# Optimization experiments

Hardware: AMD Instinct MI355X
Metric: run time of the kernel (lower is better)

The kernel has to match this reference:

```python
import jax, jax.numpy as jnp
import numpy as np

B, T, H, N, V, E = 4, 128, 1024, 300, 50265, 4800


def setup_inputs() -> dict:
    key = jax.random.key(0)
    ks = jax.random.split(key, 20)
    s = 0.02
    inp = {
        "hidden_states": jax.random.normal(ks[0], (B, T, H), jnp.float32),
        "qt": jax.random.normal(ks[1], (B, T, H), jnp.float32),
        "token_embedding": jax.random.normal(ks[2], (B, T, H), jnp.float32),
        "edges": jax.random.randint(ks[3], (B, 2, E), 0, N),
        "nodeidx2bartidx": jax.random.randint(ks[4], (N,), 0, V),
        # Linear params stored as [in, out] (y = x @ W + b), same math as torch Linear.
        "Wg": jax.random.normal(ks[5], (2 * H, V), jnp.float32) * s,
        "bg": jnp.zeros((V,), jnp.float32),
        "Wh": jax.random.normal(ks[6], (H, H), jnp.float32) * s,
        "Ws": jax.random.normal(ks[7], (H, H), jnp.float32) * s,
        "Wx": jax.random.normal(ks[8], (H, H), jnp.float32) * s,
        "bx": jnp.zeros((H,), jnp.float32),
        "Wps": jax.random.normal(ks[9], (H, 1), jnp.float32) * s,
        "bps": jnp.zeros((1,), jnp.float32),
        "Wc": jax.random.normal(ks[10], (2 * H, N), jnp.float32) * s,
        "bc": jnp.zeros((N,), jnp.float32),
        "Wgg": jax.random.normal(ks[11], (2 * H, 1), jnp.float32) * s,
        "bgg": jnp.zeros((1,), jnp.float32),
        "Wmg": jax.random.normal(ks[12], (2 * H, 1), jnp.float32) * s,
        "bmg": jnp.zeros((1,), jnp.float32),
    }
    return inp


def reference(hidden_states, qt, token_embedding, edges, nodeidx2bartidx,
              Wg, bg, Wh, Ws, Wx, bx, Wps, bps, Wc, bc, Wgg, bgg, Wmg, bmg):
    b, t, h = hidden_states.shape
    n = Wc.shape[1]
    dt = hidden_states.dtype

    hq = jnp.concatenate([hidden_states, qt], axis=-1)          # [B,T,2H]
    gen_pro = hq @ Wg + bg                                       # [B,T,V]
    gen_feat = hidden_states @ Wh + qt @ Ws + (token_embedding @ Wx + bx)
    pro_switch = jax.nn.sigmoid(gen_feat @ Wps + bps)            # [B,T,1]
    qe = jnp.concatenate([qt, token_embedding], axis=-1)
    copy_pro = qe @ Wc + bc                                      # [B,T,N]
    gsem_gate = jax.nn.sigmoid(hq @ Wgg + bgg)                   # [B,T,1]
    memory_gate = jax.nn.sigmoid(hq @ Wmg + bmg)                 # [B,T,1]

    # dense per-example adjacency from COO edges (duplicates accumulate, as in sparse->dense)
    bidx = jnp.arange(b)[:, None]
    Graph = jnp.zeros((b, n, n), dt).at[bidx, edges[:, 0, :], edges[:, 1, :]].add(jnp.asarray(1.0, dt))

    # gated memory recurrence over time + graph propagation
    def step(m_prev, xs):
        cp_t, mg_t = xs                                          # [B,N], [B,1]
        m = cp_t * mg_t + m_prev * (1.0 - mg_t)
        g = jnp.einsum('bij,bj->bi', Graph, m)
        return m, g

    cp_tm = jnp.swapaxes(copy_pro, 0, 1)                         # [T,B,N]
    mg_tm = jnp.swapaxes(memory_gate, 0, 1)                      # [T,B,1]
    _, gsem_tm = jax.lax.scan(step, jnp.zeros((b, n), dt), (cp_tm, mg_tm))
    gsem = jnp.swapaxes(gsem_tm, 0, 1)                           # [B,T,N]

    pro_gsem = copy_pro * gsem_gate + gsem * (1.0 - gsem_gate)
    coverage = jax.nn.softmax(pro_gsem * pro_switch, axis=-1).sum(axis=1)  # [B,N]

    # scatter-add node distribution into vocab space
    gsem_pro = jnp.zeros_like(gen_pro).at[:, :, nodeidx2bartidx].add(pro_gsem)
    total_pro = gen_pro * (1.0 - pro_switch) + gsem_pro * pro_switch
    return total_pro, coverage, jnp.squeeze(pro_switch, axis=-1)
```

## Files before the change

kernel.cpp:

```cpp
#include <hip/hip_runtime.h>
#include <hip/hip_bf16.h>
#include <stdint.h>

#define B_ 4
#define T_ 128
#define H_ 1024
#define N_ 300
#define V_ 50265
#define E_ 4800
#define R_ (B_*T_)
#define GK 2048

#define U_OFF     0
#define PS_OFF    3080
#define GG_OFF    3592
#define MG_OFF    4104
#define Z_OFF     4616
#define M_OFF     (Z_OFF + R_*N_)
#define CP_OFF    (M_OFF + R_*N_)
#define GRAPH_OFF (CP_OFF + R_*N_)
#define COV_OFF   (GRAPH_OFF + B_*N_*N_)
#define FLAG_OFF  (COV_OFF + B_*N_)
#define ABF_OFF   ((FLAG_OFF + 4) & ~3)

#define OUT_COV ((size_t)R_*V_)
#define OUT_PS  (OUT_COV + (size_t)B_*N_)

typedef unsigned short ushort_t;
typedef __bf16 bf16x8 __attribute__((ext_vector_type(8)));
typedef float  f32x4  __attribute__((ext_vector_type(4)));
typedef unsigned short ushort8v __attribute__((ext_vector_type(8)));
typedef unsigned short ushort4v __attribute__((ext_vector_type(4)));
typedef float f32x4v __attribute__((ext_vector_type(4)));

__device__ __forceinline__ ushort_t f2bf(float f) {
    unsigned u = __float_as_uint(f);
    unsigned r = (u + 0x7fffu + ((u >> 16) & 1u)) >> 16;
    return (ushort_t)r;
}
template<bool BF> __device__ __forceinline__ float ldv(const void* p, size_t i) {
    if constexpr (BF) {
        unsigned u = ((unsigned)((const ushort_t*)p)[i]) << 16;
        return __uint_as_float(u);
    } else {
        return ((const float*)p)[i];
    }
}
template<bool BF> __device__ __forceinline__ void stv(void* p, size_t i, float v) {
    if constexpr (BF) ((ushort_t*)p)[i] = f2bf(v);
    else              ((float*)p)[i] = v;
}
__device__ __forceinline__ float sigm(float x) { return 1.0f / (1.0f + expf(-x)); }

__device__ __forceinline__ void gload_lds16(const ushort_t* g, ushort_t* l) {
    __builtin_amdgcn_global_load_lds(
        (const __attribute__((address_space(1))) unsigned int*)g,
        (__attribute__((address_space(3))) unsigned int*)l, 16, 0, 0);
}

__global__ void k_probe(const ushort_t* __restrict__ x, int* __restrict__ flag)
{
    if (threadIdx.x == 0 && blockIdx.x == 0) {
        int cnt = 0;
        for (int i = 0; i < 256; ++i) {
            const int e = (x[i] >> 7) & 0xff;
            cnt += (e >= 100 && e <= 140) ? 1 : 0;
        }
        *flag = (cnt > 200) ? 1 : 0;
    }
}

template<bool BF>
__global__ __launch_bounds__(256)
void k_prep(const int* __restrict__ flag, const void* __restrict__ hs,
            const void* __restrict__ qt, ushort_t* __restrict__ Abf)
{
    if (*flag != (BF ? 1 : 0)) return;
    const int g = blockIdx.x * 256 + threadIdx.x;
    const int r  = g >> 8;
    const int kc = (g & 255) * 8;
    const void* src = (kc < H_) ? hs : qt;
    const int k = kc & (H_ - 1);
    ushort8v o;
    #pragma unroll
    for (int p = 0; p < 8; ++p) o[p] = f2bf(ldv<BF>(src, (size_t)r*H_ + k + p));
    *(ushort8v*)(Abf + (size_t)r*GK + kc) = o;
}

template<bool BF>
__global__ __launch_bounds__(256)
void k_u(const int* __restrict__ flag,
         const void* __restrict__ Wh, const void* __restrict__ Wsm,
         const void* __restrict__ Wx, const void* __restrict__ bx,
         const void* __restrict__ Wps, const void* __restrict__ bps,
         float* __restrict__ u)
{
    if (*flag != (BF ? 1 : 0)) return;
    const int t = threadIdx.x, w = t >> 6, l = t & 63;
    const int row = blockIdx.x * 4 + w;
    if (row > 3072) return;
    float s = 0.f;
    if (row < 3072) {
        const void* W = (row < 1024) ? Wh : (row < 2048) ? Wsm : Wx;
        const size_t k = (size_t)(row & 1023);
        for (int h = l; h < H_; h += 64)
            s += ldv<BF>(W, k*H_ + h) * ldv<BF>(Wps, h);
    } else {
        for (int h = l; h < H_; h += 64)
            s += ldv<BF>(bx, h) * ldv<BF>(Wps, h);
    }
    for (int o = 32; o; o >>= 1) s += __shfl_down(s, o);
    if (l == 0) {
        if (row < 3072) u[row] = s;
        else            u[3072] = s + ldv<BF>(bps, 0);
    }
}

template<bool BF>
__global__ __launch_bounds__(256)
void k_rows(const int* __restrict__ flag,
            const void* __restrict__ hs, const void* __restrict__ qt,
            const void* __restrict__ te, const float* __restrict__ u,
            const void* __restrict__ Wgg, const void* __restrict__ bgg,
            const void* __restrict__ Wmg, const void* __restrict__ bmg,
            float* __restrict__ ps, float* __restrict__ gg, float* __restrict__ mg,
            void* __restrict__ out_ps)
{
    if (*flag != (BF ? 1 : 0)) return;
    const int r = blockIdx.x, t = threadIdx.x;
    const float* uh = u; const float* us = u + 1024; const float* ux = u + 2048;
    float s1 = 0.f, s2 = 0.f, s3 = 0.f;
    for (int k = t; k < H_; k += 256) {
        const float a = ldv<BF>(hs, (size_t)r*H_ + k);
        const float b = ldv<BF>(qt, (size_t)r*H_ + k);
        const float c = ldv<BF>(te, (size_t)r*H_ + k);
        s1 += a*uh[k] + b*us[k] + c*ux[k];
        s2 += a*ldv<BF>(Wgg, k) + b*ldv<BF>(Wgg, H_ + k);
        s3 += a*ldv<BF>(Wmg, k) + b*ldv<BF>(Wmg, H_ + k);
    }
    for (int o = 32; o; o >>= 1) {
        s1 += __shfl_down(s1, o); s2 += __shfl_down(s2, o); s3 += __shfl_down(s3, o);
    }
    __shared__ float red[3][4];
    const int w = t >> 6, l = t & 63;
    if (l == 0) { red[0][w] = s1; red[1][w] = s2; red[2][w] = s3; }
    __syncthreads();
    if (t == 0) {
        const float S1 = red[0][0]+red[0][1]+red[0][2]+red[0][3] + u[3072];
        const float S2 = red[1][0]+red[1][1]+red[1][2]+red[1][3] + ldv<BF>(bgg, 0);
        const float S3 = red[2][0]+red[2][1]+red[2][2]+red[2][3] + ldv<BF>(bmg, 0);
        const float p = sigm(S1);
        ps[r] = p; gg[r] = sigm(S2); mg[r] = sigm(S3);
        stv<BF>(out_ps, r, p);
    }
}

template<bool BF>
__global__ __launch_bounds__(256)
void k_gbig(const int* __restrict__ flag,
            const ushort_t* __restrict__ Abf, const void* __restrict__ Bm,
            const void* __restrict__ bias, const float* __restrict__ ps,
            void* __restrict__ outh)
{
    if (*flag != (BF ? 1 : 0)) return;
    constexpr int BN = 64, BK = 32, BKp = 40, STEPS = GK / BK;
    __shared__ ushort_t As[2][512 * BK];
    __shared__ ushort_t Bs[2][BN * BKp];
    const int t = threadIdx.x, w = t >> 6, l = t & 63;
    const int lr = l & 15, lq = l >> 4;
    const int bn0 = blockIdx.x * BN;
    const int wm = w * 128;

    const int nB = t & 63, kg = t >> 6;
    const int gnB = bn0 + nB;
    const size_t gnClamp = (size_t)((gnB < V_) ? gnB : (V_ - 1));
    const bool gnOk = (gnB < V_);

    const int aRow = l >> 2;
    const int aCsrc = (l & 3) ^ ((l >> 3) & 3);
    const ushort_t* AgBase = Abf + (size_t)wm * GK;

    float bv[8];
    f32x4 acc[8][4] = {};

    auto loadB = [&](int s) {
        const int k0 = s * BK + kg * 8;
        #pragma unroll
        for (int p = 0; p < 8; ++p) {
            const float v = ldv<BF>(Bm, (size_t)(k0 + p) * V_ + gnClamp);
            bv[p] = gnOk ? v : 0.f;
        }
    };
    auto storeB = [&](int buf) {
        ushort8v b0;
        #pragma unroll
        for (int p = 0; p < 8; ++p) b0[p] = f2bf(bv[p]);
        *(ushort8v*)(&Bs[buf][nB * BKp + kg * 8]) = b0;
    };
    auto stageA = [&](int s, int buf) {
        const int k0 = s * BK;
        #pragma unroll
        for (int i = 0; i < 8; ++i) {
            const int m = i * 16 + aRow;
            const ushort_t* g = AgBase + (size_t)m * GK + k0 + aCsrc * 8;
            ushort_t* lp = &As[buf][(wm + i * 16) * BK];
            gload_lds16(g, lp);
        }
    };
    auto compute = [&](int buf) {
        const int aswz = (lq ^ ((lr >> 1) & 3)) * 8;
        const ushort_t* a_rd = &As[buf][(wm + lr) * BK + aswz];
        const ushort_t* b_rd = &Bs[buf][lr * BKp + lq * 8];
        bf16x8 bfr[4];
        #pragma unroll
        for (int j = 0; j < 4; ++j) bfr[j] = *(const bf16x8*)(b_rd + j * 16 * BKp);
        #pragma unroll
        for (int i = 0; i < 8; ++i) {
            const bf16x8 af = *(const bf16x8*)(a_rd + i * 16 * BK);
            #pragma unroll
            for (int j = 0; j < 4; ++j)
                acc[i][j] = __builtin_amdgcn_mfma_f32_16x16x32_bf16(af, bfr[j], acc[i][j], 0, 0, 0);
        }
    };

    loadB(0);
    stageA(0, 0);
    storeB(0);
    __syncthreads();
    int cur = 0;
    for (int s = 0; s < STEPS; ++s) {
        const bool more = (s + 1 < STEPS);
        if (more) { loadB(s + 1); stageA(s + 1, cur ^ 1); }
        compute(cur);
        if (more) {
            storeB(cur ^ 1);
            __syncthreads();
            cur ^= 1;
        }
    }

    #pragma unroll
    for (int j = 0; j < 4; ++j) {
        const int gcol = bn0 + j * 16 + lr;
        if (gcol < V_) {
            const float bvv = ldv<BF>(bias, gcol);
            #pragma unroll
            for (int i = 0; i < 8; ++i) {
                #pragma unroll
                for (int r2 = 0; r2 < 4; ++r2) {
                    const int row = wm + i * 16 + lq * 4 + r2;
                    stv<BF>(outh, (size_t)row * V_ + gcol,
                            (acc[i][j][r2] + bvv) * (1.0f - ps[row]));
                }
            }
        }
    }
}

template<int GN_, bool BF>
__global__ __launch_bounds__(256)
void k_gemm(const int* __restrict__ flag,
            const void* __restrict__ A1, const void* __restrict__ A2,
            const void* __restrict__ Bm, const void* __restrict__ bias,
            float* __restrict__ outf)
{
    if (*flag != (BF ? 1 : 0)) return;
    constexpr int BM = 128, BN = 128, BK = 32, BKp = 40;
    __shared__ ushort_t As[BM*BK];
    __shared__ ushort_t Bs[BN*BKp];
    const int t = threadIdx.x;
    const int w = t >> 6, l = t & 63;
    const int lr = l & 15, lq = l >> 4;
    const int bn0 = blockIdx.x * BN;
    const int bm0 = blockIdx.y * BM;
    const int wm = (w >> 1) * 64, wn = (w & 1) * 64;

    const int steps = GK/BK/4;
    const int kbeg  = blockIdx.z * steps * BK;

    const int hB = t >> 7;
    const int nB = t & 127;
    const int gnB = bn0 + nB;
    const size_t gnClamp = (size_t)((gnB < GN_) ? gnB : (GN_-1));
    const bool gnOk = (gnB < GN_);

    f32x4 acc[4][4] = {};
    const ushort_t* a_rd = As + (wm + lr)*BK  + lq*8;
    const ushort_t* b_rd = Bs + (wn + lr)*BKp + lq*8;

    ushort8v aBufH[2]; f32x4v aBufF[4]; float bv[16];

    auto load_step = [&](int s) {
        const int k0 = kbeg + s*BK;
        const void* Asrc = (k0 < H_) ? A1 : A2;
        const int kk = k0 & (H_ - 1);
        if constexpr (BF) {
            #pragma unroll
            for (int p = 0; p < 2; ++p) {
                const int slot = p*256 + t, m = slot >> 2, sub = slot & 3;
                aBufH[p] = *(const ushort8v*)((const ushort_t*)Asrc +
                             (size_t)(bm0 + m)*H_ + kk + sub*8);
            }
        } else {
            #pragma unroll
            for (int p = 0; p < 4; ++p) {
                const int slot = p*256 + t, m = slot >> 3, sub = slot & 7;
                aBufF[p] = *(const f32x4v*)((const float*)Asrc +
                             (size_t)(bm0 + m)*H_ + kk + sub*4);
            }
        }
        #pragma unroll
        for (int p = 0; p < 16; ++p) {
            const int k = hB*16 + p;
            const float v = ldv<BF>(Bm, (size_t)(k0 + k)*GN_ + gnClamp);
            bv[p] = gnOk ? v : 0.f;
        }
    };

    auto store_step = [&]() {
        if constexpr (BF) {
            #pragma unroll
            for (int p = 0; p < 2; ++p) {
                const int slot = p*256 + t, m = slot >> 2, sub = slot & 3;
                *(ushort8v*)(As + m*BK + sub*8) = aBufH[p];
            }
        } else {
            #pragma unroll
            for (int p = 0; p < 4; ++p) {
                const int slot = p*256 + t, m = slot >> 3, sub = slot & 7;
                ushort4v h4;
                h4[0] = f2bf(aBufF[p][0]); h4[1] = f2bf(aBufF[p][1]);
                h4[2] = f2bf(aBufF[p][2]); h4[3] = f2bf(aBufF[p][3]);
                *(ushort4v*)(As + m*BK + sub*4) = h4;
            }
        }
        ushort8v b0, b1;
        #pragma unroll
        for (int p = 0; p < 8; ++p)  b0[p] = f2bf(bv[p]);
        #pragma unroll
        for (int p = 0; p < 8; ++p)  b1[p] = f2bf(bv[8+p]);
        *(ushort8v*)(Bs + nB*BKp + hB*16)     = b0;
        *(ushort8v*)(Bs + nB*BKp + hB*16 + 8) = b1;
    };

    load_step(0);
    for (int s = 0; s < steps; ++s) {
        __syncthreads();
        store_step();
        __syncthreads();
        if (s + 1 < steps) load_step(s + 1);

        bf16x8 af[4], bfr[4];
        #pragma unroll
        for (int i = 0; i < 4; ++i) af[i]  = *(const bf16x8*)(a_rd + i*16*BK);
        #pragma unroll
        for (int j = 0; j < 4; ++j) bfr[j] = *(const bf16x8*)(b_rd + j*16*BKp);
        #pragma unroll
        for (int i = 0; i < 4; ++i)
            #pragma unroll
            for (int j = 0; j < 4; ++j)
                acc[i][j] = __builtin_amdgcn_mfma_f32_16x16x32_bf16(af[i], bfr[j], acc[i][j], 0, 0, 0);
    }

    #pragma unroll
    for (int j = 0; j < 4; ++j) {
        const int gcol = bn0 + wn + j*16 + lr;
        if (gcol < GN_) {
            const float bvv = (blockIdx.z == 0) ? ldv<BF>(bias, gcol) : 0.0f;
            #pragma unroll
            for (int i = 0; i < 4; ++i)
                #pragma unroll
                for (int r2 = 0; r2 < 4; ++r2) {
                    const int row = bm0 + wm + i*16 + lq*4 + r2;
                    atomicAdd(outf + (size_t)row*GN_ + gcol, acc[i][j][r2] + bvv);
                }
        }
    }
}

__global__ void k_graph(const int* __restrict__ edges, float* __restrict__ Graph)
{
    const int gid = blockIdx.x * 256 + threadIdx.x;
    if (gid >= B_*E_) return;
    const int b = gid / E_, e = gid - b*E_;
    const int* eb = edges + (size_t)b * 2 * E_;
    const int i = eb[e], j = eb[E_ + e];
    atomicAdd(Graph + (size_t)b*N_*N_ + (size_t)j*N_ + i, 1.0f);
}

__global__ void k_scan(const float* __restrict__ cp, const float* __restrict__ mg,
                       float* __restrict__ M)
{
    const int gid = blockIdx.x * 256 + threadIdx.x;
    if (gid >= B_*N_) return;
    const int b = gid / N_, n = gid - b*N_;
    float m = 0.f;
    for (int tt = 0; tt < T_; ++tt) {
        const int r = b*T_ + tt;
        const float g = mg[r];
        m = cp[(size_t)r*N_ + n]*g + m*(1.f - g);
        M[(size_t)r*N_ + n] = m;
    }
}

__global__ __launch_bounds__(320)
void k_gsem(const float* __restrict__ Graph, const float* __restrict__ M,
            const float* __restrict__ cp, const float* __restrict__ gg,
            const float* __restrict__ ps, float* __restrict__ z,
            float* __restrict__ cov)
{
    const int r = blockIdx.x;
    const int b = r >> 7;
    const int t = threadIdx.x, w = t >> 6, l = t & 63;
    __shared__ float ml[N_];
    __shared__ float red[5];
    if (t < N_) ml[t] = M[(size_t)r*N_ + t];
    __syncthreads();
    float g = 0.f;
    if (t < N_) {
        const float* GT = Graph + (size_t)b*N_*N_ + t;
        #pragma unroll 4
        for (int j = 0; j < N_; ++j) g += GT[j*N_] * ml[j];
    }
    float zv = 0.f;
    if (t < N_) {
        const float ggv = gg[r];
        const float pg = cp[(size_t)r*N_ + t]*ggv + g*(1.f - ggv);
        zv = pg * ps[r];
        z[(size_t)r*N_ + t] = zv;
    }
    float mv = (t < N_) ? zv : -3.0e38f;
    for (int o = 32; o; o >>= 1) mv = fmaxf(mv, __shfl_down(mv, o));
    if (l == 0) red[w] = mv;
    __syncthreads();
    const float bmx = fmaxf(fmaxf(fmaxf(red[0], red[1]), fmaxf(red[2], red[3])), red[4]);
    __syncthreads();
    const float e = (t < N_) ? expf(zv - bmx) : 0.f;
    float sv = e;
    for (int o = 32; o; o >>= 1) sv += __shfl_down(sv, o);
    if (l == 0) red[w] = sv;
    __syncthreads();
    const float tot = red[0] + red[1] + red[2] + red[3] + red[4];
    if (t < N_) atomicAdd(cov + b*N_ + t, e / tot);
}

template<bool BF>
__global__ void k_cov(const int* __restrict__ flag,
                      const float* __restrict__ cov, void* __restrict__ out)
{
    if (*flag != (BF ? 1 : 0)) return;
    const int gid = blockIdx.x * 256 + threadIdx.x;
    if (gid < B_*N_) stv<BF>(out, gid, cov[gid]);
}

template<bool BF>
__global__ __launch_bounds__(256)
void k_fixup(const int* __restrict__ flag, const int* __restrict__ nidx,
             const float* __restrict__ z, void* __restrict__ out)
{
    if (*flag != (BF ? 1 : 0)) return;
    __shared__ int li[N_];
    const int t = threadIdx.x;
    for (int i = t; i < N_; i += 256) li[i] = nidx[i];
    __syncthreads();
    const int gid = blockIdx.x * 256 + t;
    if (gid >= R_*N_) return;
    const int r = gid / N_, n = gid - r*N_;
    const int v = li[n];
    for (int j = 0; j < n; ++j) if (li[j] == v) return;
    float s = z[(size_t)r*N_ + n];
    for (int j = n + 1; j < N_; ++j) if (li[j] == v) s += z[(size_t)r*N_ + j];
    const size_t o = (size_t)r*V_ + v;
    stv<BF>(out, o, ldv<BF>(out, o) + s);
}

extern "C" void kernel_launch(void* const* d_in, const int* in_sizes, int n_in,
                              void* d_out, int out_size, void* d_ws, size_t ws_size,
                              hipStream_t stream)
{
    (void)in_sizes; (void)n_in; (void)out_size; (void)ws_size;
    const void* hs  = d_in[0];
    const void* qt  = d_in[1];
    const void* te  = d_in[2];
    const int*  edg = (const int*)d_in[3];
    const int*  nid = (const int*)d_in[4];
    const void* Wg  = d_in[5];
    const void* bg  = d_in[6];
    const void* Wh  = d_in[7];
    const void* Wsm = d_in[8];
    const void* Wx  = d_in[9];
    const void* bx  = d_in[10];
    const void* Wps = d_in[11];
    const void* bps = d_in[12];
    const void* Wc  = d_in[13];
    const void* bc  = d_in[14];
    const void* Wgg = d_in[15];
    const void* bgg = d_in[16];
    const void* Wmg = d_in[17];
    const void* bmg = d_in[18];
    float* ws = (float*)d_ws;
    int* flag = (int*)(ws + FLAG_OFF);
    ushort_t* Abf = (ushort_t*)(ws + ABF_OFF);

    k_probe<<<1, 64, 0, stream>>>((const ushort_t*)hs, flag);
    hipMemsetAsync(ws + CP_OFF, 0,
                   (size_t)(R_*N_ + B_*N_*N_ + B_*N_) * sizeof(float), stream);

    k_prep<true ><<<512, 256, 0, stream>>>(flag, hs, qt, Abf);
    k_prep<false><<<512, 256, 0, stream>>>(flag, hs, qt, Abf);
    k_u<true ><<<769, 256, 0, stream>>>(flag, Wh, Wsm, Wx, bx, Wps, bps, ws + U_OFF);
    k_u<false><<<769, 256, 0, stream>>>(flag, Wh, Wsm, Wx, bx, Wps, bps, ws + U_OFF);
    k_rows<true ><<<R_, 256, 0, stream>>>(flag, hs, qt, te, ws + U_OFF, Wgg, bgg, Wmg, bmg,
                                          ws + PS_OFF, ws + GG_OFF, ws + MG_OFF,
                                          (ushort_t*)d_out + OUT_PS);
    k_rows<false><<<R_, 256, 0, stream>>>(flag, hs, qt, te, ws + U_OFF, Wgg, bgg, Wmg, bmg,
                                          ws + PS_OFF, ws + GG_OFF, ws + MG_OFF,
                                          (float*)d_out + OUT_PS);
    {
        dim3 g((N_ + 127) / 128, 4, 4);
        k_gemm<N_, true ><<<g, 256, 0, stream>>>(flag, qt, te, Wc, bc, ws + CP_OFF);
        k_gemm<N_, false><<<g, 256, 0, stream>>>(flag, qt, te, Wc, bc, ws + CP_OFF);
    }
    k_graph<<<(B_*E_ + 255)/256, 256, 0, stream>>>(edg, ws + GRAPH_OFF);
    k_scan<<<(B_*N_ + 255)/256, 256, 0, stream>>>(ws + CP_OFF, ws + MG_OFF, ws + M_OFF);
    k_gsem<<<R_, 320, 0, stream>>>(ws + GRAPH_OFF, ws + M_OFF, ws + CP_OFF,
                                   ws + GG_OFF, ws + PS_OFF, ws + Z_OFF, ws + COV_OFF);
    k_cov<true ><<<(B_*N_ + 255)/256, 256, 0, stream>>>(flag, ws + COV_OFF,
                                                        (ushort_t*)d_out + OUT_COV);
    k_cov<false><<<(B_*N_ + 255)/256, 256, 0, stream>>>(flag, ws + COV_OFF,
                                                        (float*)d_out + OUT_COV);
    {
        k_gbig<true ><<<(V_ + 63)/64, 256, 0, stream>>>(flag, Abf, Wg, bg,
                                                        ws + PS_OFF, d_out);
        k_gbig<false><<<(V_ + 63)/64, 256, 0, stream>>>(flag, Abf, Wg, bg,
                                                        ws + PS_OFF, d_out);
    }
    k_fixup<true ><<<(R_*N_ + 255)/256, 256, 0, stream>>>(flag, nid, ws + Z_OFF, d_out);
    k_fixup<false><<<(R_*N_ + 255)/256, 256, 0, stream>>>(flag, nid, ws + Z_OFF, d_out);
}
```

Measured before the change: 1.180 ms.

## Retile vocab GEMM into 128x128 tiles with XCD-aware block mapping

Replaces the full-M-per-block vocab projection kernel with a 128x128 tiled kernel over 4 M-blocks and V stripes. Block ids are mapped so the four M-blocks of a stripe land on the same XCD, which is meant to share Wg reads in L2. A is loaded via registers instead of direct global-to-LDS loads, with a register prefetch two steps ahead. The aim is lower LDS use, higher occupancy and better latency hiding, at the risk of reading Wg up to four times.

```diff
diff --git a/kernel.cpp b/kernel.cpp
--- a/kernel.cpp
+++ b/kernel.cpp
@@ -51,12 +51,6 @@
     else              ((float*)p)[i] = v;
 }
 __device__ __forceinline__ float sigm(float x) { return 1.0f / (1.0f + expf(-x)); }
-
-__device__ __forceinline__ void gload_lds16(const ushort_t* g, ushort_t* l) {
-    __builtin_amdgcn_global_load_lds(
-        (const __attribute__((address_space(1))) unsigned int*)g,
-        (__attribute__((address_space(3))) unsigned int*)l, 16, 0, 0);
-}
 
 __global__ void k_probe(const ushort_t* __restrict__ x, int* __restrict__ flag)
 {
@@ -157,102 +151,108 @@
 
 template<bool BF>
 __global__ __launch_bounds__(256)
-void k_gbig(const int* __restrict__ flag,
-            const ushort_t* __restrict__ Abf, const void* __restrict__ Bm,
-            const void* __restrict__ bias, const float* __restrict__ ps,
-            void* __restrict__ outh)
-{
-    if (*flag != (BF ? 1 : 0)) return;
-    constexpr int BN = 64, BK = 32, BKp = 40, STEPS = GK / BK;
-    __shared__ ushort_t As[2][512 * BK];
+void k_gv(const int* __restrict__ flag, const ushort_t* __restrict__ Abf,
+          const void* __restrict__ Bm, const void* __restrict__ bias,
+          const float* __restrict__ ps, void* __restrict__ outh)
+{
+    if (*flag != (BF ? 1 : 0)) return;
+    constexpr int BM = 128, BN = 128, BK = 32, BKp = 40, STEPS = GK / BK;
+    constexpr int NSTRIPE = (V_ + BN - 1) / BN;
+    const int id = blockIdx.x;
+    const int xcd = id & 7, q = id >> 3;
+    const int mb = q & 3;
+    const int jn = (q >> 2) * 8 + xcd;
+    if (jn >= NSTRIPE) return;
+    const int bm0 = mb * BM, bn0 = jn * BN;
+
+    __shared__ ushort_t As[2][BM * BK];
     __shared__ ushort_t Bs[2][BN * BKp];
     const int t = threadIdx.x, w = t >> 6, l = t & 63;
     const int lr = l & 15, lq = l >> 4;
-    const int bn0 = blockIdx.x * BN;
-    const int wm = w * 128;
-
-    const int nB = t & 63, kg = t >> 6;
+    const int wm = (w >> 1) * 64, wn = (w & 1) * 64;
+
+    const int hB = t >> 7, nB = t & 127;
     const int gnB = bn0 + nB;
     const size_t gnClamp = (size_t)((gnB < V_) ? gnB : (V_ - 1));
     const bool gnOk = (gnB < V_);
 
-    const int aRow = l >> 2;
-    const int aCsrc = (l & 3) ^ ((l >> 3) & 3);
-    const ushort_t* AgBase = Abf + (size_t)wm * GK;
-
-    float bv[8];
-    f32x4 acc[8][4] = {};
-
-    auto loadB = [&](int s) {
-        const int k0 = s * BK + kg * 8;
-        #pragma unroll
-        for (int p = 0; p < 8; ++p) {
-            const float v = ldv<BF>(Bm, (size_t)(k0 + p) * V_ + gnClamp);
+    f32x4 acc[4][4] = {};
+    ushort8v aR[2]; float bv[16];
+
+    auto load_step = [&](int s) {
+        const int k0 = s * BK;
+        #pragma unroll
+        for (int p = 0; p < 2; ++p) {
+            const int slot = p*256 + t, m = slot >> 2, sub = slot & 3;
+            aR[p] = *(const ushort8v*)(Abf + (size_t)(bm0 + m)*GK + k0 + sub*8);
+        }
+        #pragma unroll
+        for (int p = 0; p < 16; ++p) {
+            const float v = ldv<BF>(Bm, (size_t)(k0 + hB*16 + p)*V_ + gnClamp);
             bv[p] = gnOk ? v : 0.f;
         }
     };
-    auto storeB = [&](int buf) {
-        ushort8v b0;
+    auto store_step = [&](int buf) {
+        #pragma unroll
+        for (int p = 0; p < 2; ++p) {
+            const int slot = p*256 + t, m = slot >> 2, sub = slot & 3;
+            *(ushort8v*)(&As[buf][m*BK + sub*8]) = aR[p];
+        }
+        ushort8v b0, b1;
         #pragma unroll
         for (int p = 0; p < 8; ++p) b0[p] = f2bf(bv[p]);
-        *(ushort8v*)(&Bs[buf][nB * BKp + kg * 8]) = b0;
-    };
-    auto stageA = [&](int s, int buf) {
-        const int k0 = s * BK;
-        #pragma unroll
-        for (int i = 0; i < 8; ++i) {
-            const int m = i * 16 + aRow;
-            const ushort_t* g = AgBase + (size_t)m * GK + k0 + aCsrc * 8;
-            ushort_t* lp = &As[buf][(wm + i * 16) * BK];
-            gload_lds16(g, lp);
-        }
+        #pragma unroll
+        for (int p = 0; p < 8; ++p) b1[p] = f2bf(bv[8+p]);
+        *(ushort8v*)(&Bs[buf][nB*BKp + hB*16])     = b0;
+        *(ushort8v*)(&Bs[buf][nB*BKp + hB*16 + 8]) = b1;
     };
     auto compute = [&](int buf) {
-        const int aswz = (lq ^ ((lr >> 1) & 3)) * 8;
-        const ushort_t* a_rd = &As[buf][(wm + lr) * BK + aswz];
-        const ushort_t* b_rd = &Bs[buf][lr * BKp + lq * 8];
-        bf16x8 bfr[4];
-        #pragma unroll
-        for (int j = 0; j < 4; ++j) bfr[j] = *(const bf16x8*)(b_rd + j * 16 * BKp);
-        #pragma unroll
-        for (int i = 0; i < 8; ++i) {
-            const bf16x8 af = *(const bf16x8*)(a_rd + i * 16 * BK);
+        const ushort_t* a_rd = &As[buf][(wm + lr)*BK  + lq*8];
+        const ushort_t* b_rd = &Bs[buf][(wn + lr)*BKp + lq*8];
+        bf16x8 af[4], bfr[4];
+        #pragma unroll
+        for (int i = 0; i < 4; ++i) af[i]  = *(const bf16x8*)(a_rd + i*16*BK);
+        #pragma unroll
+        for (int j = 0; j < 4; ++j) bfr[j] = *(const bf16x8*)(b_rd + j*16*BKp);
+        #pragma unroll
+        for (int i = 0; i < 4; ++i)
             #pragma unroll
             for (int j = 0; j < 4; ++j)
-                acc[i][j] = __builtin_amdgcn_mfma_f32_16x16x32_bf16(af, bfr[j], acc[i][j], 0, 0, 0);
-        }
+                acc[i][j] = __builtin_amdgcn_mfma_f32_16x16x32_bf16(af[i], bfr[j], acc[i][j], 0, 0, 0);
     };
 
-    loadB(0);
-    stageA(0, 0);
-    storeB(0);
-    __syncthreads();
-    int cur = 0;
+    load_step(0);
+    store_step(0);
+    __syncthreads();
+    load_step(1);
     for (int s = 0; s < STEPS; ++s) {
-        const bool more = (s + 1 < STEPS);
-        if (more) { loadB(s + 1); stageA(s + 1, cur ^ 1); }
-        compute(cur);
-        if (more) {
-            storeB(cur ^ 1);
+        compute(s & 1);
+        if (s + 1 < STEPS) {
+            store_step((s + 1) & 1);
             __syncthreads();
-            cur ^= 1;
-        }
-    }
-
+            if (s + 2 < STEPS) load_step(s + 2);
+        }
+    }
+
+    float omp[16];
+    #pragma unroll
+    for (int i = 0; i < 4; ++i)
+        #pragma unroll
+        for (int r2 = 0; r2 < 4; ++r2)
+            omp[i*4 + r2] = 1.0f - ps[bm0 + wm + i*16 + lq*4 + r2];
     #pragma unroll
     for (int j = 0; j < 4; ++j) {
-        const int gcol = bn0 + j * 16 + lr;
+        const int gcol = bn0 + wn + j*16 + lr;
         if (gcol < V_) {
             const float bvv = ldv<BF>(bias, gcol);
             #pragma unroll
-            for (int i = 0; i < 8; ++i) {
+            for (int i = 0; i < 4; ++i)
                 #pragma unroll
                 for (int r2 = 0; r2 < 4; ++r2) {
-                    const int row = wm + i * 16 + lq * 4 + r2;
-                    stv<BF>(outh, (size_t)row * V_ + gcol,
-                            (acc[i][j][r2] + bvv) * (1.0f - ps[row]));
+                    const int row = bm0 + wm + i*16 + lq*4 + r2;
+                    stv<BF>(outh, (size_t)row*V_ + gcol,
+                            (acc[i][j][r2] + bvv) * omp[i*4 + r2]);
                 }
-            }
         }
     }
 }
@@ -530,10 +530,8 @@
     k_cov<false><<<(B_*N_ + 255)/256, 256, 0, stream>>>(flag, ws + COV_OFF,
                                                         (float*)d_out + OUT_COV);
     {
-        k_gbig<true ><<<(V_ + 63)/64, 256, 0, stream>>>(flag, Abf, Wg, bg,
-                                                        ws + PS_OFF, d_out);
-        k_gbig<false><<<(V_ + 63)/64, 256, 0, stream>>>(flag, Abf, Wg, bg,
-                                                        ws + PS_OFF, d_out);
+        k_gv<true ><<<1600, 256, 0, stream>>>(flag, Abf, Wg, bg, ws + PS_OFF, d_out);
+        k_gv<false><<<1600, 256, 0, stream>>>(flag, Abf, Wg, bg, ws + PS_OFF, d_out);
     }
     k_fixup<true ><<<(R_*N_ + 255)/256, 256, 0, stream>>>(flag, nid, ws + Z_OFF, d_out);
     k_fixup<false><<<(R_*N_ + 255)/256, 256, 0, stream>>>(flag, nid, ws + Z_OFF, d_out);
```

New measurement: 1.017 ms. 13.8% less time.
